# Kernel tuning notes

Measured on AMD Instinct MI355X. Metric: run time of the kernel, lower is better.

## Reference

```python
import jax, jax.numpy as jnp
import numpy as np

N = 8388608          # total items across all scopes
SEG = 64             # uniform scope (segment) length
TARGET_MAX = 1000000


def setup_inputs() -> dict:
    key = jax.random.key(0)
    k1, k2, k3 = jax.random.split(key, 3)
    mean = jax.random.normal(k1, (N, 1), dtype=jnp.float32)
    variance = jax.random.uniform(k2, (N, 1), dtype=jnp.float32)
    targets = jax.random.randint(k3, (N,), 0, TARGET_MAX, dtype=jnp.int64)
    return {"mean": mean, "variance": variance, "targets": targets, "scope": SEG}


def reference(mean, variance, targets, scope):
    # score = cat(mean, variance) -> column 0 is mean m, column 1 is variance v
    n = mean.shape[0]
    b = n // scope                                   # number of ragged segments (uniform here)
    m = mean[:, 0].reshape(b, scope)
    v = variance[:, 0].reshape(b, scope)
    t = targets.reshape(b, scope)

    # per-segment descending sort by targets
    idx = jnp.argsort(-t, axis=1)                    # [b, scope]
    ms = jnp.take_along_axis(m, idx, axis=1)
    vs = jnp.take_along_axis(v, idx, axis=1)

    # tril(exp(m_i - m_j + (v_i + v_j)/2)).sum(0)[j]
    #   = exp(-m_j + v_j/2) * sum_{i>=j} exp(m_i + v_i/2)
    z = jnp.exp(ms + 0.5 * vs)                       # [b, scope]
    rev_cumsum = jnp.cumsum(z[:, ::-1], axis=1)[:, ::-1]  # sum over i >= j
    logS = -ms + 0.5 * vs + jnp.log(rev_cumsum)      # -log(1/S) = log S

    per_seg_loss = jnp.mean(logS, axis=1)            # torch.mean over the segment
    avg = jnp.sum(per_seg_loss) / b                  # losses / len(scope)
    return avg.reshape(1)                            # matches torch.Tensor([0]) accumulator shape
```

## Files before the change

### kernel.cpp

```cpp
#include <hip/hip_runtime.h>

#define N_TOTAL 8388608
#define SEG 64
#define NSEG (N_TOTAL / SEG)
#define NPAIR (NSEG / 2)
#define TPB 256
#define BLOCKS 4096
#define WAVES (BLOCKS * TPB / 64)
#define ITERS (NPAIR / WAVES)

template <int CTRL>
__device__ __forceinline__ unsigned dpp_qp(unsigned v) {
    return (unsigned)__builtin_amdgcn_update_dpp(0, (int)v, CTRL, 0xf, 0xf, true);
}
template <int CTRL, int ROW_MASK>
__device__ __forceinline__ float dpp_add(float x) {
    int mv = __builtin_amdgcn_update_dpp(0, __float_as_int(x), CTRL, ROW_MASK, 0xf, true);
    return x + __int_as_float(mv);
}
template <int D>
__device__ __forceinline__ unsigned lane_xor_c(unsigned v) {
    if (D == 1) return dpp_qp<0xB1>(v);
    if (D == 2) return dpp_qp<0x4E>(v);
    return (unsigned)__shfl_xor((int)v, D, 64);
}

__global__ __launch_bounds__(TPB) void mledis_seg2(
    const float2* __restrict__ mean2,
    const float2* __restrict__ var2,
    const int2*   __restrict__ tgt2,
    float* __restrict__ partial)
{
    const int lane = threadIdx.x & 63;
    const int h    = lane >> 5;
    const int l5   = lane & 31;
    const int waveId = blockIdx.x * (TPB / 64) + (threadIdx.x >> 6);

    float2 m[ITERS], v[ITERS];
    int2   t[ITERS];
    #pragma unroll
    for (int it = 0; it < ITERS; ++it) {
        const int base2 = (waveId + it * WAVES) * 64 + h * 32 + l5;
        m[it] = mean2[base2];
        v[it] = var2[base2];
        t[it] = tgt2[base2];
    }

    float acc = 0.0f;

    #pragma unroll
    for (int it = 0; it < ITERS; ++it) {
        const float z0 = __expf(fmaf(0.5f, v[it].x, m[it].x));
        const float z1 = __expf(fmaf(0.5f, v[it].y, m[it].y));
        acc += fmaf(0.5f, v[it].x, -m[it].x) + fmaf(0.5f, v[it].y, -m[it].y);

        const unsigned e0 = 2u * (unsigned)l5;
        unsigned k0 = (((unsigned)t[it].x) << 6) | (63u - e0);
        unsigned k1 = (((unsigned)t[it].y) << 6) | (63u - (e0 + 1u));

        #define CMP_XLANE(K, D)                                              \
            {                                                                \
                const unsigned o0 = lane_xor_c<D>(k0);                       \
                const unsigned o1 = lane_xor_c<D>(k1);                       \
                const bool lower = (l5 & (D)) == 0;                          \
                const bool up    = (l5 & ((K) >> 1)) == 0;                   \
                const bool sel   = (up == lower);                            \
                const unsigned mn0 = min(k0, o0), mx0 = max(k0, o0);         \
                const unsigned mn1 = min(k1, o1), mx1 = max(k1, o1);         \
                k0 = sel ? mn0 : mx0;                                        \
                k1 = sel ? mn1 : mx1;                                        \
            }
        #define CMP_LOCAL(K)                                                 \
            {                                                                \
                const bool up = (l5 & ((K) >> 1)) == 0;                      \
                const unsigned mn = min(k0, k1), mx = max(k0, k1);           \
                k0 = up ? mn : mx;                                           \
                k1 = up ? mx : mn;                                           \
            }
        CMP_LOCAL(2)
        CMP_XLANE(4, 1)  CMP_LOCAL(4)
        CMP_XLANE(8, 2)  CMP_XLANE(8, 1)  CMP_LOCAL(8)
        CMP_XLANE(16, 4) CMP_XLANE(16, 2) CMP_XLANE(16, 1) CMP_LOCAL(16)
        CMP_XLANE(32, 8) CMP_XLANE(32, 4) CMP_XLANE(32, 2) CMP_XLANE(32, 1) CMP_LOCAL(32)
        CMP_XLANE(64, 16) CMP_XLANE(64, 8) CMP_XLANE(64, 4) CMP_XLANE(64, 2) CMP_XLANE(64, 1) CMP_LOCAL(64)
        #undef CMP_XLANE
        #undef CMP_LOCAL

        const int o0i = 63 - (int)(k0 & 63u);
        const int o1i = 63 - (int)(k1 & 63u);
        const int a0 = (h * 32 + (o0i >> 1)) << 2;
        const int a1 = (h * 32 + (o1i >> 1)) << 2;
        const int zi0 = __float_as_int(z0);
        const int zi1 = __float_as_int(z1);
        const float g00 = __int_as_float(__builtin_amdgcn_ds_bpermute(a0, zi0));
        const float g01 = __int_as_float(__builtin_amdgcn_ds_bpermute(a0, zi1));
        const float g10 = __int_as_float(__builtin_amdgcn_ds_bpermute(a1, zi0));
        const float g11 = __int_as_float(__builtin_amdgcn_ds_bpermute(a1, zi1));
        const float za0 = (o0i & 1) ? g01 : g00;
        const float za1 = (o1i & 1) ? g11 : g10;

        float P = za0 + za1;
        P = dpp_add<0x111, 0xf>(P);
        P = dpp_add<0x112, 0xf>(P);
        P = dpp_add<0x114, 0xf>(P);
        P = dpp_add<0x118, 0xf>(P);
        P = dpp_add<0x142, 0xa>(P);
        acc += __logf(P) + __logf(P - za1);
    }

    #pragma unroll
    for (int off = 32; off > 0; off >>= 1)
        acc += __shfl_xor(acc, off, 64);

    __shared__ float sacc[TPB / 64];
    const int waveInBlock = threadIdx.x >> 6;
    if (lane == 0) sacc[waveInBlock] = acc;
    __syncthreads();
    if (threadIdx.x == 0) {
        float b = 0.0f;
        #pragma unroll
        for (int i = 0; i < TPB / 64; ++i) b += sacc[i];
        partial[blockIdx.x] = b;
    }
}

__global__ __launch_bounds__(TPB) void mledis_final_reduce(
    const float* __restrict__ partial, float* __restrict__ out)
{
    float s = 0.0f;
    for (int i = threadIdx.x; i < BLOCKS; i += TPB) s += partial[i];
    #pragma unroll
    for (int off = 32; off > 0; off >>= 1) s += __shfl_xor(s, off, 64);

    __shared__ float sacc[TPB / 64];
    const int lane = threadIdx.x & 63;
    const int w = threadIdx.x >> 6;
    if (lane == 0) sacc[w] = s;
    __syncthreads();
    if (threadIdx.x == 0) {
        float tot = 0.0f;
        #pragma unroll
        for (int i = 0; i < TPB / 64; ++i) tot += sacc[i];
        out[0] = tot * (1.0f / (float)N_TOTAL);
    }
}

extern "C" void kernel_launch(void* const* d_in, const int* in_sizes, int n_in,
                              void* d_out, int out_size, void* d_ws, size_t ws_size,
                              hipStream_t stream) {
    const float2* mean2 = (const float2*)d_in[0];
    const float2* var2  = (const float2*)d_in[1];
    const int2*   tgt2  = (const int2*)d_in[2];

    float* partial = (float*)d_ws;
    float* out = (float*)d_out;

    mledis_seg2<<<BLOCKS, TPB, 0, stream>>>(mean2, var2, tgt2, partial);
    mledis_final_reduce<<<1, TPB, 0, stream>>>(partial, out);
}
```

Baseline: 126.4 us.

## Halve grid, software-pipeline loads, use ds_swizzle and fuse logs

Halves the block count so each wave handles twice as many segment pairs, and swaps the load-everything-upfront scheme for a one-iteration-ahead prefetch to save registers. Cross-lane xor for distances 4, 8 and 16 moves from shfl to ds_swizzle, the kernel gets a launch-bounds occupancy hint, and the two logs become one log of a product. Risks: fewer blocks may leave the GPU underfilled, and merging the logs could lose precision or overflow.

Measured after the change: 122.1 us. -3.4%, faster.

```diff
diff --git a/kernel.cpp b/kernel.cpp
--- a/kernel.cpp
+++ b/kernel.cpp
@@ -5,7 +5,7 @@
 #define NSEG (N_TOTAL / SEG)
 #define NPAIR (NSEG / 2)
 #define TPB 256
-#define BLOCKS 4096
+#define BLOCKS 2048
 #define WAVES (BLOCKS * TPB / 64)
 #define ITERS (NPAIR / WAVES)
 
@@ -22,10 +22,10 @@
 __device__ __forceinline__ unsigned lane_xor_c(unsigned v) {
     if (D == 1) return dpp_qp<0xB1>(v);
     if (D == 2) return dpp_qp<0x4E>(v);
-    return (unsigned)__shfl_xor((int)v, D, 64);
+    return (unsigned)__builtin_amdgcn_ds_swizzle((int)v, (D << 10) | 0x1F);
 }
 
-__global__ __launch_bounds__(TPB) void mledis_seg2(
+__global__ __launch_bounds__(TPB, 8) void mledis_seg2(
     const float2* __restrict__ mean2,
     const float2* __restrict__ var2,
     const int2*   __restrict__ tgt2,
@@ -36,27 +36,27 @@
     const int l5   = lane & 31;
     const int waveId = blockIdx.x * (TPB / 64) + (threadIdx.x >> 6);
 
-    float2 m[ITERS], v[ITERS];
-    int2   t[ITERS];
-    #pragma unroll
-    for (int it = 0; it < ITERS; ++it) {
-        const int base2 = (waveId + it * WAVES) * 64 + h * 32 + l5;
-        m[it] = mean2[base2];
-        v[it] = var2[base2];
-        t[it] = tgt2[base2];
-    }
+    float2 mc = mean2[waveId * 64 + lane];
+    float2 vc = var2 [waveId * 64 + lane];
+    int2   tc = tgt2 [waveId * 64 + lane];
 
     float acc = 0.0f;
 
     #pragma unroll
     for (int it = 0; it < ITERS; ++it) {
-        const float z0 = __expf(fmaf(0.5f, v[it].x, m[it].x));
-        const float z1 = __expf(fmaf(0.5f, v[it].y, m[it].y));
-        acc += fmaf(0.5f, v[it].x, -m[it].x) + fmaf(0.5f, v[it].y, -m[it].y);
+        float2 mn_, vn_; int2 tn_;
+        if (it + 1 < ITERS) {
+            const int b = (waveId + (it + 1) * WAVES) * 64 + lane;
+            mn_ = mean2[b]; vn_ = var2[b]; tn_ = tgt2[b];
+        }
+
+        const float z0 = __expf(fmaf(0.5f, vc.x, mc.x));
+        const float z1 = __expf(fmaf(0.5f, vc.y, mc.y));
+        acc += fmaf(0.5f, vc.x, -mc.x) + fmaf(0.5f, vc.y, -mc.y);
 
         const unsigned e0 = 2u * (unsigned)l5;
-        unsigned k0 = (((unsigned)t[it].x) << 6) | (63u - e0);
-        unsigned k1 = (((unsigned)t[it].y) << 6) | (63u - (e0 + 1u));
+        unsigned k0 = (((unsigned)tc.x) << 6) | (63u - e0);
+        unsigned k1 = (((unsigned)tc.y) << 6) | (63u - (e0 + 1u));
 
         #define CMP_XLANE(K, D)                                              \
             {                                                                \
@@ -105,7 +105,9 @@
         P = dpp_add<0x114, 0xf>(P);
         P = dpp_add<0x118, 0xf>(P);
         P = dpp_add<0x142, 0xa>(P);
-        acc += __logf(P) + __logf(P - za1);
+        acc += __logf(P * (P - za1));
+
+        mc = mn_; vc = vn_; tc = tn_;
     }
 
     #pragma unroll
```
